# Optimization experiments

Measured on AMD Instinct MI355X. Metric: run time of the kernel, lower is better.

## Reference

```python
import jax, jax.numpy as jnp
import numpy as np


def setup_inputs() -> dict:
    key = jax.random.key(0)
    k1, k2 = jax.random.split(key)
    B, D, H, W = 8, 64, 384, 512
    input1 = jax.random.normal(k1, (B, D, H, W), dtype=jnp.float32)
    input2 = jax.random.normal(k2, (B, 2, H, W), dtype=jnp.float32)  # flow (u, v) in pixels
    return {"input1": input1, "input2": input2}


def reference(input1, input2):
    # Equivalent of: grid = base_grid + 2*flow/(size-1); F.grid_sample(input1, grid,
    # mode='bilinear', padding_mode='border', align_corners=True).
    # With align_corners=True the normalized grid unmaps exactly to pixel coords
    # fx = x + u, fy = y + v; border padding clips coords to the image rectangle.
    B, D, H, W = input1.shape
    dt = input1.dtype
    u = input2[:, 0]  # (B, H, W) horizontal flow
    v = input2[:, 1]  # (B, H, W) vertical flow

    fx = jnp.arange(W, dtype=dt)[None, None, :] + u
    fy = jnp.arange(H, dtype=dt)[None, :, None] + v
    # padding_mode='border': clip sample coordinates to valid range
    fx = jnp.clip(fx, 0.0, W - 1)
    fy = jnp.clip(fy, 0.0, H - 1)

    x0 = jnp.floor(fx)
    y0 = jnp.floor(fy)
    wx = fx - x0  # bilinear weights, (B, H, W)
    wy = fy - y0
    x0i = x0.astype(jnp.int32)
    y0i = y0.astype(jnp.int32)
    x1i = jnp.minimum(x0i + 1, W - 1)
    y1i = jnp.minimum(y0i + 1, H - 1)

    img = jnp.transpose(input1, (0, 2, 3, 1))  # (B, H, W, D) channels-last for gather
    bidx = jnp.arange(B)[:, None, None]

    def gather(yi, xi):
        return img[bidx, yi, xi]  # (B, H, W, D)

    out = (gather(y0i, x0i) * ((1 - wy) * (1 - wx))[..., None]
           + gather(y0i, x1i) * ((1 - wy) * wx)[..., None]
           + gather(y1i, x0i) * (wy * (1 - wx))[..., None]
           + gather(y1i, x1i) * (wy * wx)[..., None])
    return jnp.transpose(out, (0, 3, 1, 2))  # back to (B, D, H, W)
```

## Files before the change

### kernel.cpp

```cpp
#include <hip/hip_runtime.h>

#define Bdim 8
#define Ddim 64
#define Hdim 384
#define Wdim 512

__global__ __launch_bounds__(256) void resample2d_kernel(
    const float* __restrict__ img,
    const float* __restrict__ flow,
    float* __restrict__ out)
{
    const int HW = Hdim * Wdim;
    int idx = blockIdx.x * blockDim.x + threadIdx.x;
    if (idx >= Bdim * HW) return;

    int w  = idx % Wdim;
    int hw = idx % HW;
    int h  = hw / Wdim;
    int b  = idx / HW;

    float u = flow[(size_t)b * 2 * HW + hw];
    float v = flow[(size_t)b * 2 * HW + HW + hw];

    float fx = fminf(fmaxf((float)w + u, 0.0f), (float)(Wdim - 1));
    float fy = fminf(fmaxf((float)h + v, 0.0f), (float)(Hdim - 1));
    float x0f = floorf(fx);
    float y0f = floorf(fy);
    float wx = fx - x0f;
    float wy = fy - y0f;
    int x0 = (int)x0f;
    int y0 = (int)y0f;
    int x1 = min(x0 + 1, Wdim - 1);
    int y1 = min(y0 + 1, Hdim - 1);

    float w00 = (1.0f - wy) * (1.0f - wx);
    float w01 = (1.0f - wy) * wx;
    float w10 = wy * (1.0f - wx);
    float w11 = wy * wx;

    int i00 = y0 * Wdim + x0;
    int i01 = y0 * Wdim + x1;
    int i10 = y1 * Wdim + x0;
    int i11 = y1 * Wdim + x1;

    const float* base  = img + (size_t)b * Ddim * HW;
    float*       obase = out + (size_t)b * Ddim * HW + hw;

    #pragma unroll 4
    for (int d = 0; d < Ddim; ++d) {
        const float* p = base + (size_t)d * HW;
        float r = p[i00] * w00 + p[i01] * w01 + p[i10] * w10 + p[i11] * w11;
        obase[(size_t)d * HW] = r;
    }
}

extern "C" void kernel_launch(void* const* d_in, const int* in_sizes, int n_in,
                              void* d_out, int out_size, void* d_ws, size_t ws_size,
                              hipStream_t stream) {
    const float* img  = (const float*)d_in[0];
    const float* flow = (const float*)d_in[1];
    float* out = (float*)d_out;

    const int total = Bdim * Hdim * Wdim;
    dim3 block(256);
    dim3 grid((total + block.x - 1) / block.x);
    resample2d_kernel<<<grid, block, 0, stream>>>(img, flow, out);
}
```

Measured before the change: 877.3 us.

## Tile blocks as 4x64 pixel patches, batch gathers, and use nontemporal flow/output access

Each block now covers a 4-row by 64-column 2D tile instead of 256 consecutive pixels on one row. Neighbouring rows share source pixels, so gathers from the same block should get more cache reuse. The channel loop issues 32 gather loads per group of 8 channels before computing, which gives more memory-level parallelism. Flow loads and output stores are marked nontemporal to keep them out of the cache, and launch bounds ask for 8 blocks per CU. The extra in-flight loads raise register pressure, which may limit occupancy.

```diff
diff --git a/kernel.cpp b/kernel.cpp
--- a/kernel.cpp
+++ b/kernel.cpp
@@ -5,22 +5,36 @@
 #define Hdim 384
 #define Wdim 512
 
-__global__ __launch_bounds__(256) void resample2d_kernel(
+#define TH 4
+#define TW 64
+#define TILES_W (Wdim / TW)
+#define TILES_H (Hdim / TH)
+#define TILES_PER_B (TILES_W * TILES_H)
+
+
+__global__ __launch_bounds__(256, 8) void resample2d_kernel(
     const float* __restrict__ img,
     const float* __restrict__ flow,
     float* __restrict__ out)
 {
     const int HW = Hdim * Wdim;
-    int idx = blockIdx.x * blockDim.x + threadIdx.x;
-    if (idx >= Bdim * HW) return;
 
-    int w  = idx % Wdim;
-    int hw = idx % HW;
-    int h  = hw / Wdim;
-    int b  = idx / HW;
+    int bid = blockIdx.x;
+    int b   = bid / TILES_PER_B;
+    int s   = bid - b * TILES_PER_B;
+    int th  = s >> 3;
+    int tw  = s & 7;
 
-    float u = flow[(size_t)b * 2 * HW + hw];
-    float v = flow[(size_t)b * 2 * HW + HW + hw];
+    int lane = threadIdx.x & 63;
+    int wv   = threadIdx.x >> 6;
+
+    int h  = th * TH + wv;
+    int w  = tw * TW + lane;
+    int hw = h * Wdim + w;
+
+    const float* fb = flow + (size_t)b * 2 * HW;
+    float u = __builtin_nontemporal_load(fb + hw);
+    float v = __builtin_nontemporal_load(fb + HW + hw);
 
     float fx = fminf(fmaxf((float)w + u, 0.0f), (float)(Wdim - 1));
     float fy = fminf(fmaxf((float)h + v, 0.0f), (float)(Hdim - 1));
@@ -43,14 +57,25 @@
     int i10 = y1 * Wdim + x0;
     int i11 = y1 * Wdim + x1;
 
-    const float* base  = img + (size_t)b * Ddim * HW;
-    float*       obase = out + (size_t)b * Ddim * HW + hw;
+    const float* ib = img + (size_t)b * Ddim * HW;
+    float*       ob = out + (size_t)b * Ddim * HW;
 
-    #pragma unroll 4
-    for (int d = 0; d < Ddim; ++d) {
-        const float* p = base + (size_t)d * HW;
-        float r = p[i00] * w00 + p[i01] * w01 + p[i10] * w10 + p[i11] * w11;
-        obase[(size_t)d * HW] = r;
+    for (int d0 = 0; d0 < Ddim; d0 += 8) {
+        float v00[8], v01[8], v10[8], v11[8];
+        #pragma unroll
+        for (int dd = 0; dd < 8; ++dd) {
+            const float* p = ib + (size_t)(d0 + dd) * HW;
+            v00[dd] = p[i00];
+            v01[dd] = p[i01];
+            v10[dd] = p[i10];
+            v11[dd] = p[i11];
+        }
+        #pragma unroll
+        for (int dd = 0; dd < 8; ++dd) {
+            float r = v00[dd] * w00 + v01[dd] * w01
+                    + v10[dd] * w10 + v11[dd] * w11;
+            __builtin_nontemporal_store(r, ob + (size_t)(d0 + dd) * HW + hw);
+        }
     }
 }
 
@@ -61,8 +86,8 @@
     const float* flow = (const float*)d_in[1];
     float* out = (float*)d_out;
 
-    const int total = Bdim * Hdim * Wdim;
+    const int total_blocks = Bdim * TILES_PER_B;
     dim3 block(256);
-    dim3 grid((total + block.x - 1) / block.x);
+    dim3 grid(total_blocks);
     resample2d_kernel<<<grid, block, 0, stream>>>(img, flow, out);
 }
```

Result: faster. 819.9 us (-6.5%).
